# Kernel optimization log

Hardware: AMD Instinct MI355X
Metric: run time of the kernel (lower is better)

Reference implementation:

```python
import jax, jax.numpy as jnp
import numpy as np
from jax import lax

UP = 2          # upsampling factor
K = 3           # conv kernel size
PADDING = K // 2
CLAMP = 256.0   # conv_clamp
ACT_GAIN = float(np.sqrt(2.0))  # lrelu def_gain
LRELU_SLOPE = 0.2
_F1 = np.array([1.0, 3.0, 3.0, 1.0], np.float32)
_F1 = _F1 / _F1.sum()  # upfirdn2d.setup_filter normalizes to sum 1


def setup_inputs() -> dict:
    key = jax.random.key(0)
    k1, k2 = jax.random.split(key)
    x = jax.random.normal(k1, (8, 512, 64, 64), jnp.float32)
    weight = jax.random.normal(k2, (256, 512, K, K), jnp.float32)
    bias = jnp.zeros((256,), jnp.float32)
    return {"x": x, "weight": weight, "bias": bias}


def reference(x, weight, bias):
    O, I, kh, kw = weight.shape
    w = weight * (1.0 / np.sqrt(I * kh * kw))  # weight_gain

    # --- conv2d_resample fast path for up=2, kernel>1 ---
    # base padding px0=px1=py0=py1=PADDING, then up>1 adjustments
    fw = _F1.shape[0]
    p0 = PADDING + (fw + UP - 1) // 2
    p1 = PADDING + (fw - UP) // 2
    p0 -= kw - 1
    p1 -= kw - UP
    pt = max(min(-p0, -p1), 0)
    # torch.conv_transpose2d(x, w.transpose(0,1), stride=UP, padding=pt), no weight flip
    # == input-dilated convolution with spatially flipped kernel, pad (k-1-pt)
    y = lax.conv_general_dilated(
        x, jnp.flip(w, (2, 3)),
        window_strides=(1, 1),
        padding=[(kh - 1 - pt, kh - 1 - pt), (kw - 1 - pt, kw - 1 - pt)],
        lhs_dilation=(UP, UP),
        dimension_numbers=('NCHW', 'OIHW', 'NCHW'))  # [N, O, 2H+k-2, 2W+k-2]

    # upfirdn2d: pad (p0+pt, p1+pt) per side, depthwise FIR, gain = up**2
    f2 = jnp.asarray(np.outer(_F1, _F1) * (UP ** 2), jnp.float32)  # [4,4], symmetric
    fk = jnp.broadcast_to(f2[None, None], (O, 1, fw, fw))
    pad = (p0 + pt, p1 + pt)
    y = lax.conv_general_dilated(
        y, fk, (1, 1), padding=[pad, pad],
        dimension_numbers=('NCHW', 'OIHW', 'NCHW'),
        feature_group_count=O)  # [N, O, 2H, 2W]

    # --- bias_act: bias + lrelu * gain, clamp ---
    y = y + bias[None, :, None, None]
    y = jnp.where(y >= 0, y, LRELU_SLOPE * y) * ACT_GAIN
    y = jnp.clip(y, -CLAMP, CLAMP)
    return y
```

## Files before the change

### kernel.cpp

```cpp
#include <hip/hip_runtime.h>
#include <hip/hip_fp16.h>
#include <cstdint>
#include <cmath>


typedef _Float16 f16;
typedef _Float16 f16x8 __attribute__((ext_vector_type(8)));
typedef float f32x4 __attribute__((ext_vector_type(4)));

#define GLD16(g, l)                                                            \
  __builtin_amdgcn_global_load_lds(                                            \
      (const __attribute__((address_space(1))) void*)(g),                      \
      (__attribute__((address_space(3))) void*)(l), 16, 0, 0)

#define BAR()                                                                  \
  {                                                                            \
    __asm__ volatile("" ::: "memory");                                         \
    __builtin_amdgcn_s_barrier();                                              \
    __asm__ volatile("" ::: "memory");                                         \
  }
#define VMCNT(n) __asm__ volatile("s_waitcnt vmcnt(" #n ")" ::: "memory")

static const size_t XP_ELEMS = (size_t)8 * 66 * 66 * 512;
static const size_t XP_BYTES = XP_ELEMS * 2;
static const size_t WEFF_ELEMS = (size_t)9 * 1024 * 512;
static const size_t WEFF_BYTES = WEFF_ELEMS * 2;

__global__ __launch_bounds__(256) void ring_zero(f16* __restrict__ xp) {
  int g = blockIdx.x * 256 + threadIdx.x;
  int n = g / 16640, r = g % 16640;
  int seg = r >> 6, c8 = r & 63;
  int y, xc;
  if (seg < 66) {
    y = 0; xc = seg;
  } else if (seg < 132) {
    y = 65; xc = seg - 66;
  } else {
    int rem = seg - 132;
    y = 1 + (rem >> 1);
    xc = (rem & 1) * 65;
  }
  f16x8 z = {0, 0, 0, 0, 0, 0, 0, 0};
  *(f16x8*)&xp[((size_t)((n * 66 + y) * 66 + xc) << 9) + (c8 << 3)] = z;
}

__global__ __launch_bounds__(256) void pad_transpose(const float* __restrict__ x,
                                                     f16* __restrict__ xp) {
  __shared__ f16 tile[64][132];
  const int b = blockIdx.x;
  const int cq = b & 3, h = (b >> 2) & 63, n = b >> 8;
  const int t = threadIdx.x;
  const int c0 = cq << 7;
#pragma unroll
  for (int r = 0; r < 32; ++r) {
    int idx = r * 256 + t;
    int cl = idx >> 6, w = idx & 63;
    float v = x[(((size_t)(n * 512 + c0 + cl) * 64 + h) << 6) + w];
    tile[w][cl] = (f16)v;
  }
  __syncthreads();
#pragma unroll
  for (int q = 0; q < 4; ++q) {
    int ch = q * 256 + t;
    int w = ch >> 4, cc = ch & 15;
    f16x8 v = *(const f16x8*)&tile[w][cc << 3];
    *(f16x8*)&xp[((size_t)((n * 66 + h + 1) * 66 + w + 1) << 9) + c0 + (cc << 3)] = v;
  }
}

__global__ __launch_bounds__(256) void weff_kernel(const float* __restrict__ w,
                                                   f16* __restrict__ weff) {
  const int g = blockIdx.x * 256 + threadIdx.x;
  const int o = g >> 9, c = g & 511;
  const float* wp = w + (size_t)(o * 512 + c) * 9;
  float w9[9];
#pragma unroll
  for (int k = 0; k < 9; ++k) w9[k] = wp[k];
  const float f0 = 0.25f, f1 = 0.75f, f2 = 0.75f, f3 = 0.25f;
  const float G[2][3][3] = {
      {{0.f, f0, f1}, {f1, f2, f3}, {f3, 0.f, 0.f}},
      {{0.f, 0.f, f0}, {f0, f1, f2}, {f2, f3, 0.f}}};
  const float scale = 64.f / sqrtf(512.f * 9.f);
#pragma unroll
  for (int py = 0; py < 2; ++py)
#pragma unroll
    for (int dy = 0; dy < 3; ++dy) {
      float ty[3];
#pragma unroll
      for (int bx = 0; bx < 3; ++bx)
        ty[bx] = w9[bx] * G[py][dy][0] + w9[3 + bx] * G[py][dy][1] +
                 w9[6 + bx] * G[py][dy][2];
#pragma unroll
      for (int px = 0; px < 2; ++px)
#pragma unroll
        for (int dx = 0; dx < 3; ++dx) {
          float v = ty[0] * G[px][dx][0] + ty[1] * G[px][dx][1] +
                    ty[2] * G[px][dx][2];
          int s = dy * 3 + dx;
          int col = (o << 2) | (py << 1) | px;
          weff[((size_t)(s * 1024 + col) << 9) + c] = (f16)(v * scale);
        }
    }
}

__global__ __launch_bounds__(512, 2) void conv_main(const f16* __restrict__ xp,
                                                    const f16* __restrict__ weff,
                                                    const float* __restrict__ bias,
                                                    float* __restrict__ out) {
  __shared__ f16 lds[65536];
  f16* A0 = lds;
  f16* A1 = lds + 16384;
  f16* B0 = lds + 32768;
  f16* B1 = lds + 49152;

  const int t = threadIdx.x;
  const int lane = t & 63, wave = t >> 6;
  const int wm = wave >> 2, wn = wave & 3;
  const int lrow = lane & 15, kgrp = lane >> 4;

  const int d = blockIdx.x;
  const int xcd = d & 7, idx = d >> 3;
  const int ntile = xcd >> 1;
  const int mtile = ((xcd & 1) << 6) + idx;
  const int n_img = mtile >> 4;
  const int i0 = (mtile & 15) << 2;
  const int col0 = ntile << 8;

  const int c_swz = ((t & 7) ^ ((t >> 3) & 7)) << 3;
  const int jj = t >> 3;
  const f16* sA[2][2];
  const f16* sB[2][2];
#pragma unroll
  for (int q = 0; q < 2; ++q)
#pragma unroll
    for (int h = 0; h < 2; ++h) {
      sA[q][h] = xp + ((size_t)((n_img * 66 + i0 + h * 2 + q) * 66 + jj) << 9) + c_swz;
      sB[q][h] = weff + ((size_t)(col0 + h * 128 + q * 64 + jj) << 9) + c_swz;
    }

#define ST_A(buf, h, off)                                     \
  {                                                           \
    GLD16(sA[0][h] + (off), (buf) + (h)*8192 + t * 8);        \
    GLD16(sA[1][h] + (off), (buf) + (h)*8192 + 4096 + t * 8); \
  }
#define ST_B(buf, h, off)                                     \
  {                                                           \
    GLD16(sB[0][h] + (off), (buf) + (h)*8192 + t * 8);        \
    GLD16(sB[1][h] + (off), (buf) + (h)*8192 + 4096 + t * 8); \
  }

#define OFFS(tt, oa, ob)                                   \
  {                                                        \
    int s_ = (tt) >> 3, kc_ = (tt)&7;                      \
    int dy_ = s_ / 3, dx_ = s_ - 3 * dy_;                  \
    oa = ((dy_ * 66 + dx_) << 9) + (kc_ << 6);             \
    ob = (s_ << 19) + (kc_ << 6);                          \
  }

  f16x8 af[4][2];
  f16x8 bf[2][2][2];
  f32x4 acc[8][4];
#pragma unroll
  for (int m = 0; m < 8; ++m)
#pragma unroll
    for (int n = 0; n < 4; ++n) {
      f32x4 z = {0.f, 0.f, 0.f, 0.f};
      acc[m][n] = z;
    }

#define LDA(bufp, mh)                                                          \
  _Pragma("unroll") for (int m = 0; m < 4; ++m) _Pragma("unroll") for (int kk = 0; kk < 2; ++kk) \
      af[m][kk] = *(const f16x8*)&(                                            \
          bufp)[((wm * 128 + (mh)*64 + m * 16 + lrow) << 6) +                  \
                ((((kk << 2) | kgrp) ^ (lrow & 7)) << 3)];

#define LDB(bufp, nh)                                                          \
  _Pragma("unroll") for (int n = 0; n < 2; ++n) _Pragma("unroll") for (int kk = 0; kk < 2; ++kk) \
      bf[nh][n][kk] = *(const f16x8*)&(                                        \
          bufp)[((wn * 64 + (nh)*32 + n * 16 + lrow) << 6) +                   \
                ((((kk << 2) | kgrp) ^ (lrow & 7)) << 3)];

#define MM(mh, nh)                                                             \
  __builtin_amdgcn_s_setprio(1);                                               \
  _Pragma("unroll") for (int kk = 0; kk < 2; ++kk)                             \
  _Pragma("unroll") for (int m = 0; m < 4; ++m)                                \
  _Pragma("unroll") for (int n = 0; n < 2; ++n)                                \
      acc[(mh)*4 + m][(nh)*2 + n] = __builtin_amdgcn_mfma_f32_16x16x32_f16(    \
          af[m][kk], bf[nh][n][kk], acc[(mh)*4 + m][(nh)*2 + n], 0, 0, 0);     \
  __builtin_amdgcn_s_setprio(0);

  {
    int oa0, ob0, oa1, ob1;
    OFFS(0, oa0, ob0);
    OFFS(1, oa1, ob1);
    ST_A(A0, 0, oa0);
    ST_A(A0, 1, oa0);
    ST_B(B0, 0, ob0);
    ST_B(B0, 1, ob0);
    ST_A(A1, 0, oa1);
    (void)ob1;
  }
  VMCNT(2);
  BAR();

  for (int j = 0; j < 36; ++j) {
    const int t1 = 2 * j + 1;
    int tn0 = t1 + 1;
    if (tn0 > 71) tn0 = 71;
    int tn1 = t1 + 2;
    if (tn1 > 71) tn1 = 71;
    int oa1, ob1, oan0, obn0, oan1, obn1;
    OFFS(t1, oa1, ob1);
    OFFS(tn0, oan0, obn0);
    OFFS(tn1, oan1, obn1);
    (void)obn1;

    LDA(A0, 0);
    LDB(B0, 0);
    ST_A(A1, 1, oa1);
    BAR();
    MM(0, 0);
    BAR();
    LDB(B0, 1);
    ST_B(B1, 0, ob1);
    BAR();
    MM(0, 1);
    BAR();
    LDA(A0, 1);
    ST_B(B1, 1, ob1);
    BAR();
    MM(1, 1);
    BAR();
    ST_A(A0, 0, oan0);
    VMCNT(2);
    BAR();
    MM(1, 0);
    BAR();
    LDA(A1, 0);
    LDB(B1, 0);
    ST_A(A0, 1, oan0);
    BAR();
    MM(0, 0);
    BAR();
    LDB(B1, 1);
    ST_B(B0, 0, obn0);
    BAR();
    MM(0, 1);
    BAR();
    LDA(A1, 1);
    ST_B(B0, 1, obn0);
    BAR();
    MM(1, 1);
    BAR();
    ST_A(A1, 0, oan1);
    VMCNT(2);
    BAR();
    MM(1, 0);
    BAR();
  }
  VMCNT(0);

  const float inv = 1.0f / 64.0f;
#pragma unroll
  for (int na = 0; na < 4; ++na) {
    const int colL = wn * 64 + na * 16 + lrow;
    const int col = col0 + colL;
    const int oG = col >> 2;
    const int py = (col >> 1) & 1, px = col & 1;
    const float bz = bias[oG];
#pragma unroll
    for (int ma = 0; ma < 8; ++ma) {
#pragma unroll
      for (int r = 0; r < 4; ++r) {
        const int rowL = wm * 128 + ma * 16 + (kgrp << 2) + r;
        const int ii = i0 + (rowL >> 6), j2 = rowL & 63;
        float v = acc[ma][na][r] * inv + bz;
        v = (v < 0.f ? 0.2f * v : v) * 1.41421356237f;
        v = fminf(fmaxf(v, -256.f), 256.f);
        out[((size_t)((n_img * 256 + oG) * 128 + (ii << 1) + py) << 7) +
            (j2 << 1) + px] = v;
      }
    }
  }
#undef ST_A
#undef ST_B
#undef OFFS
#undef LDA
#undef LDB
#undef MM
}

__global__ void naive_conv(const float* __restrict__ x, const float* __restrict__ w,
                           const float* __restrict__ bias, float* __restrict__ out) {
  size_t g = (size_t)blockIdx.x * 256 + threadIdx.x;
  const int xo = g & 127, yo = (int)((g >> 7) & 127);
  const int o = (int)((g >> 14) & 255), n = (int)(g >> 22);
  const int px = xo & 1, py = yo & 1, j = xo >> 1, i = yo >> 1;
  const float f0 = 0.25f, f1 = 0.75f, f2 = 0.75f, f3 = 0.25f;
  const float G0[3][3] = {{0.f, f0, f1}, {f1, f2, f3}, {f3, 0.f, 0.f}};
  const float G1[3][3] = {{0.f, 0.f, f0}, {f0, f1, f2}, {f2, f3, 0.f}};
  const float(*Gy)[3] = py ? G1 : G0;
  const float(*Gx)[3] = px ? G1 : G0;
  float acc = 0.f;
  for (int c = 0; c < 512; ++c) {
    const float* wp = w + ((size_t)o * 512 + c) * 9;
    float w9[9];
#pragma unroll
    for (int k = 0; k < 9; ++k) w9[k] = wp[k];
    float ty[3][3];
#pragma unroll
    for (int dy = 0; dy < 3; ++dy)
#pragma unroll
      for (int bx = 0; bx < 3; ++bx)
        ty[dy][bx] =
            w9[bx] * Gy[dy][0] + w9[3 + bx] * Gy[dy][1] + w9[6 + bx] * Gy[dy][2];
#pragma unroll
    for (int dy = 0; dy < 3; ++dy) {
      int yy = i + dy - 1;
      if (yy < 0 || yy > 63) continue;
#pragma unroll
      for (int dx = 0; dx < 3; ++dx) {
        int xx = j + dx - 1;
        if (xx < 0 || xx > 63) continue;
        float eff =
            ty[dy][0] * Gx[dx][0] + ty[dy][1] * Gx[dx][1] + ty[dy][2] * Gx[dx][2];
        acc += x[(((size_t)(n * 512 + c) * 64 + yy) << 6) + xx] * eff;
      }
    }
  }
  float v = acc * (1.f / sqrtf(512.f * 9.f)) + bias[o];
  v = (v < 0.f ? 0.2f * v : v) * 1.41421356237f;
  v = fminf(fmaxf(v, -256.f), 256.f);
  out[g] = v;
}

extern "C" void kernel_launch(void* const* d_in, const int* in_sizes, int n_in,
                              void* d_out, int out_size, void* d_ws, size_t ws_size,
                              hipStream_t stream) {
  const float* x = (const float*)d_in[0];
  const float* w = (const float*)d_in[1];
  const float* bias = (const float*)d_in[2];
  float* out = (float*)d_out;

  const size_t NEED = XP_BYTES + WEFF_BYTES;
  if (ws_size < NEED) {
    naive_conv<<<131072, 256, 0, stream>>>(x, w, bias, out);
    return;
  }
  f16* xp = (f16*)d_ws;
  f16* weff = (f16*)((char*)d_ws + XP_BYTES);

  ring_zero<<<520, 256, 0, stream>>>(xp);
  pad_transpose<<<2048, 256, 0, stream>>>(x, xp);
  weff_kernel<<<512, 256, 0, stream>>>(w, weff);
  conv_main<<<512, 512, 0, stream>>>(xp, weff, bias, out);
}
```

Measured before the change: 477.7 us.

## Merge prep kernels into one launch and issue whole-tile prefetches earlier in GEMM loop

The three preprocessing kernels (border zeroing, pad/transpose to fp16, effective-weight build) become a single launch whose block ranges dispatch to each role, cutting two kernel launches and their gaps. In the main conv loop, global-to-LDS stores for the next tile are now issued as full A and B halves together, and both buffers are primed up front. Wait counts are relaxed to vmcnt(8), so more loads are in flight before each barrier. This aims to hide global latency better, at the cost of more outstanding loads and a stricter dependency on buffer reuse ordering.

```diff
diff --git a/kernel.cpp b/kernel.cpp
--- a/kernel.cpp
+++ b/kernel.cpp
@@ -26,81 +26,82 @@
 static const size_t WEFF_ELEMS = (size_t)9 * 1024 * 512;
 static const size_t WEFF_BYTES = WEFF_ELEMS * 2;
 
-__global__ __launch_bounds__(256) void ring_zero(f16* __restrict__ xp) {
-  int g = blockIdx.x * 256 + threadIdx.x;
-  int n = g / 16640, r = g % 16640;
-  int seg = r >> 6, c8 = r & 63;
-  int y, xc;
-  if (seg < 66) {
-    y = 0; xc = seg;
-  } else if (seg < 132) {
-    y = 65; xc = seg - 66;
-  } else {
-    int rem = seg - 132;
-    y = 1 + (rem >> 1);
-    xc = (rem & 1) * 65;
-  }
-  f16x8 z = {0, 0, 0, 0, 0, 0, 0, 0};
-  *(f16x8*)&xp[((size_t)((n * 66 + y) * 66 + xc) << 9) + (c8 << 3)] = z;
-}
-
-__global__ __launch_bounds__(256) void pad_transpose(const float* __restrict__ x,
-                                                     f16* __restrict__ xp) {
+__global__ __launch_bounds__(256) void prep(const float* __restrict__ x,
+                                            const float* __restrict__ w,
+                                            f16* __restrict__ xp,
+                                            f16* __restrict__ weff) {
   __shared__ f16 tile[64][132];
   const int b = blockIdx.x;
-  const int cq = b & 3, h = (b >> 2) & 63, n = b >> 8;
   const int t = threadIdx.x;
-  const int c0 = cq << 7;
-#pragma unroll
-  for (int r = 0; r < 32; ++r) {
-    int idx = r * 256 + t;
-    int cl = idx >> 6, w = idx & 63;
-    float v = x[(((size_t)(n * 512 + c0 + cl) * 64 + h) << 6) + w];
-    tile[w][cl] = (f16)v;
-  }
-  __syncthreads();
-#pragma unroll
-  for (int q = 0; q < 4; ++q) {
-    int ch = q * 256 + t;
-    int w = ch >> 4, cc = ch & 15;
-    f16x8 v = *(const f16x8*)&tile[w][cc << 3];
-    *(f16x8*)&xp[((size_t)((n * 66 + h + 1) * 66 + w + 1) << 9) + c0 + (cc << 3)] = v;
-  }
-}
-
-__global__ __launch_bounds__(256) void weff_kernel(const float* __restrict__ w,
-                                                   f16* __restrict__ weff) {
-  const int g = blockIdx.x * 256 + threadIdx.x;
-  const int o = g >> 9, c = g & 511;
-  const float* wp = w + (size_t)(o * 512 + c) * 9;
-  float w9[9];
-#pragma unroll
-  for (int k = 0; k < 9; ++k) w9[k] = wp[k];
-  const float f0 = 0.25f, f1 = 0.75f, f2 = 0.75f, f3 = 0.25f;
-  const float G[2][3][3] = {
-      {{0.f, f0, f1}, {f1, f2, f3}, {f3, 0.f, 0.f}},
-      {{0.f, 0.f, f0}, {f0, f1, f2}, {f2, f3, 0.f}}};
-  const float scale = 64.f / sqrtf(512.f * 9.f);
-#pragma unroll
-  for (int py = 0; py < 2; ++py)
-#pragma unroll
-    for (int dy = 0; dy < 3; ++dy) {
-      float ty[3];
-#pragma unroll
-      for (int bx = 0; bx < 3; ++bx)
-        ty[bx] = w9[bx] * G[py][dy][0] + w9[3 + bx] * G[py][dy][1] +
-                 w9[6 + bx] * G[py][dy][2];
-#pragma unroll
-      for (int px = 0; px < 2; ++px)
-#pragma unroll
-        for (int dx = 0; dx < 3; ++dx) {
-          float v = ty[0] * G[px][dx][0] + ty[1] * G[px][dx][1] +
-                    ty[2] * G[px][dx][2];
-          int s = dy * 3 + dx;
-          int col = (o << 2) | (py << 1) | px;
-          weff[((size_t)(s * 1024 + col) << 9) + c] = (f16)(v * scale);
-        }
-    }
+
+  if (b < 2048) {
+    const int cq = b & 3, h = (b >> 2) & 63, n = b >> 8;
+    const int c0 = cq << 7;
+#pragma unroll
+    for (int r = 0; r < 32; ++r) {
+      int idx = r * 256 + t;
+      int cl = idx >> 6, wpos = idx & 63;
+      float v = x[(((size_t)(n * 512 + c0 + cl) * 64 + h) << 6) + wpos];
+      tile[wpos][cl] = (f16)v;
+    }
+    __syncthreads();
+#pragma unroll
+    for (int q = 0; q < 4; ++q) {
+      int ch = q * 256 + t;
+      int wpos = ch >> 4, cc = ch & 15;
+      f16x8 v = *(const f16x8*)&tile[wpos][cc << 3];
+      *(f16x8*)&xp[((size_t)((n * 66 + h + 1) * 66 + wpos + 1) << 9) + c0 +
+                   (cc << 3)] = v;
+    }
+  } else if (b < 2560) {
+    const int g = (b - 2048) * 256 + t;
+    const int o = g >> 9, c = g & 511;
+    const float* wp = w + (size_t)(o * 512 + c) * 9;
+    float w9[9];
+#pragma unroll
+    for (int k = 0; k < 9; ++k) w9[k] = wp[k];
+    const float f0 = 0.25f, f1 = 0.75f, f2 = 0.75f, f3 = 0.25f;
+    const float G[2][3][3] = {
+        {{0.f, f0, f1}, {f1, f2, f3}, {f3, 0.f, 0.f}},
+        {{0.f, 0.f, f0}, {f0, f1, f2}, {f2, f3, 0.f}}};
+    const float scale = 64.f / sqrtf(512.f * 9.f);
+#pragma unroll
+    for (int py = 0; py < 2; ++py)
+#pragma unroll
+      for (int dy = 0; dy < 3; ++dy) {
+        float ty[3];
+#pragma unroll
+        for (int bx = 0; bx < 3; ++bx)
+          ty[bx] = w9[bx] * G[py][dy][0] + w9[3 + bx] * G[py][dy][1] +
+                   w9[6 + bx] * G[py][dy][2];
+#pragma unroll
+        for (int px = 0; px < 2; ++px)
+#pragma unroll
+          for (int dx = 0; dx < 3; ++dx) {
+            float v = ty[0] * G[px][dx][0] + ty[1] * G[px][dx][1] +
+                      ty[2] * G[px][dx][2];
+            int s = dy * 3 + dx;
+            int col = (o << 2) | (py << 1) | px;
+            weff[((size_t)(s * 1024 + col) << 9) + c] = (f16)(v * scale);
+          }
+      }
+  } else {
+    int g = (b - 2560) * 256 + t;
+    int n = g / 16640, r = g % 16640;
+    int seg = r >> 6, c8 = r & 63;
+    int y, xc;
+    if (seg < 66) {
+      y = 0; xc = seg;
+    } else if (seg < 132) {
+      y = 65; xc = seg - 66;
+    } else {
+      int rem = seg - 132;
+      y = 1 + (rem >> 1);
+      xc = (rem & 1) * 65;
+    }
+    f16x8 z = {0, 0, 0, 0, 0, 0, 0, 0};
+    *(f16x8*)&xp[((size_t)((n * 66 + y) * 66 + xc) << 9) + (c8 << 3)] = z;
+  }
 }
 
 __global__ __launch_bounds__(512, 2) void conv_main(const f16* __restrict__ xp,
@@ -193,67 +194,66 @@
     int oa0, ob0, oa1, ob1;
     OFFS(0, oa0, ob0);
     OFFS(1, oa1, ob1);
+    ST_B(B0, 0, ob0);
+    ST_B(B0, 1, ob0);
     ST_A(A0, 0, oa0);
     ST_A(A0, 1, oa0);
-    ST_B(B0, 0, ob0);
-    ST_B(B0, 1, ob0);
+    ST_B(B1, 0, ob1);
+    ST_B(B1, 1, ob1);
     ST_A(A1, 0, oa1);
-    (void)ob1;
-  }
-  VMCNT(2);
+    ST_A(A1, 1, oa1);
+  }
+  VMCNT(8);
   BAR();
 
   for (int j = 0; j < 36; ++j) {
-    const int t1 = 2 * j + 1;
-    int tn0 = t1 + 1;
+    int tn0 = 2 * j + 2;
     if (tn0 > 71) tn0 = 71;
-    int tn1 = t1 + 2;
+    int tn1 = 2 * j + 3;
     if (tn1 > 71) tn1 = 71;
-    int oa1, ob1, oan0, obn0, oan1, obn1;
-    OFFS(t1, oa1, ob1);
+    int oan0, obn0, oan1, obn1;
     OFFS(tn0, oan0, obn0);
     OFFS(tn1, oan1, obn1);
-    (void)obn1;
 
     LDA(A0, 0);
     LDB(B0, 0);
-    ST_A(A1, 1, oa1);
     BAR();
     MM(0, 0);
     BAR();
     LDB(B0, 1);
-    ST_B(B1, 0, ob1);
     BAR();
     MM(0, 1);
     BAR();
     LDA(A0, 1);
-    ST_B(B1, 1, ob1);
+    ST_B(B0, 0, obn0);
+    ST_B(B0, 1, obn0);
     BAR();
     MM(1, 1);
     BAR();
     ST_A(A0, 0, oan0);
-    VMCNT(2);
+    ST_A(A0, 1, oan0);
+    VMCNT(8);
     BAR();
     MM(1, 0);
     BAR();
     LDA(A1, 0);
     LDB(B1, 0);
-    ST_A(A0, 1, oan0);
     BAR();
     MM(0, 0);
     BAR();
     LDB(B1, 1);
-    ST_B(B0, 0, obn0);
     BAR();
     MM(0, 1);
     BAR();
     LDA(A1, 1);
-    ST_B(B0, 1, obn0);
+    ST_B(B1, 0, obn1);
+    ST_B(B1, 1, obn1);
     BAR();
     MM(1, 1);
     BAR();
     ST_A(A1, 0, oan1);
-    VMCNT(2);
+    ST_A(A1, 1, oan1);
+    VMCNT(8);
     BAR();
     MM(1, 0);
     BAR();
@@ -350,8 +350,6 @@
   f16* xp = (f16*)d_ws;
   f16* weff = (f16*)((char*)d_ws + XP_BYTES);
 
-  ring_zero<<<520, 256, 0, stream>>>(xp);
-  pad_transpose<<<2048, 256, 0, stream>>>(x, xp);
-  weff_kernel<<<512, 256, 0, stream>>>(w, weff);
+  prep<<<3080, 256, 0, stream>>>(x, w, xp, weff);
   conv_main<<<512, 512, 0, stream>>>(xp, weff, bias, out);
 }
```

Result: no change. 479.7 us (+0.4%).
